# Optimization experiments

Hardware: AMD Instinct MI355X
Metric: run time of the kernel (lower is better)

Reference implementation:

```python
import jax, jax.numpy as jnp
import numpy as np

NUM_HEADS = 8
FOCUSING_FACTOR = 3.0
EPS = 1e-6


def setup_inputs() -> dict:
    key = jax.random.key(0)
    ks = jax.random.split(key, 5)
    B, C, H, W = 16, 256, 64, 64
    hd = C // NUM_HEADS
    return {
        "x": jax.random.normal(ks[0], (B, C, H, W), jnp.float32),
        "qkv_w": jax.random.normal(ks[1], (3 * C, C), jnp.float32) * 0.02,
        "qkv_b": jnp.zeros((3 * C,), jnp.float32),
        "proj_w": jax.random.normal(ks[2], (C, C), jnp.float32) * 0.02,
        "proj_b": jnp.zeros((C,), jnp.float32),
        "dwc_w": jax.random.normal(ks[3], (hd, 1, 5, 5), jnp.float32) * 0.02,
        "dwc_b": jnp.zeros((hd,), jnp.float32),
        "scale": jnp.zeros((1, 1, C), jnp.float32),
    }


def reference(x, qkv_w, qkv_b, proj_w, proj_b, dwc_w, dwc_b, scale):
    B, C, H, W = x.shape
    N = H * W
    hd = C // NUM_HEADS

    # b c h w -> b (h w) c
    xf = x.reshape(B, C, N).transpose(0, 2, 1)
    qkv = xf @ qkv_w.T + qkv_b  # [B, N, 3C]
    q, k, v = jnp.split(qkv, 3, axis=-1)

    # focusing feature map
    q = jax.nn.relu(q) + EPS
    k = jax.nn.relu(k) + EPS
    sc = jax.nn.softplus(scale)
    q = q / sc
    k = k / sc
    q_norm = jnp.linalg.norm(q, axis=-1, keepdims=True)
    k_norm = jnp.linalg.norm(k, axis=-1, keepdims=True)
    # focusing_factor <= 6 branch
    q = q ** FOCUSING_FACTOR
    k = k ** FOCUSING_FACTOR
    q = q / jnp.linalg.norm(q, axis=-1, keepdims=True) * q_norm
    k = k / jnp.linalg.norm(k, axis=-1, keepdims=True) * k_norm

    # b n (h c) -> (b h) n c
    def to_heads(t):
        return t.reshape(B, N, NUM_HEADS, hd).transpose(0, 2, 1, 3).reshape(B * NUM_HEADS, N, hd)

    q, k, v = to_heads(q), to_heads(k), to_heads(v)

    i, j, c, d = N, N, hd, hd
    z = 1.0 / (jnp.einsum('bic,bc->bi', q, k.sum(axis=1)) + EPS)
    if i * j * (c + d) > c * d * (i + j):
        kv = jnp.einsum('bjc,bjd->bcd', k, v)  # [(BH), c, d]
        out = jnp.einsum('bic,bcd,bi->bid', q, kv, z)
    else:
        qk = jnp.einsum('bic,bjc->bij', q, k)
        out = jnp.einsum('bij,bjd,bi->bid', qk, v, z)

    # depthwise conv on v: b (w h) c -> b c w h (square map)
    num = int(N ** 0.5)
    fm = v.transpose(0, 2, 1).reshape(B * NUM_HEADS, hd, num, num)
    fm = jax.lax.conv_general_dilated(
        fm, dwc_w, window_strides=(1, 1), padding='SAME',
        feature_group_count=hd,
        dimension_numbers=('NCHW', 'OIHW', 'NCHW')) + dwc_b[None, :, None, None]
    fm = fm.reshape(B * NUM_HEADS, hd, N).transpose(0, 2, 1)
    out = out + fm

    # (b h) n c -> b n (h c)
    out = out.reshape(B, NUM_HEADS, N, hd).transpose(0, 2, 1, 3).reshape(B, N, C)
    out = out @ proj_w.T + proj_b
    # b (h w) c -> b c h w
    return out.transpose(0, 2, 1).reshape(B, C, H, W)
```

## Files before the change

### kernel.cpp

```cpp
#include <hip/hip_runtime.h>
#include <cmath>

#define B_   16
#define C_   256
#define HW_  64
#define N_   4096
#define NH_  8
#define HD_  32
#define M_   (B_ * N_)
#define QKVC (3 * C_)
#define EPS_ 1e-6f

typedef short bf16x8 __attribute__((ext_vector_type(8)));
typedef float f32x4 __attribute__((ext_vector_type(4)));
typedef unsigned int u32x4 __attribute__((ext_vector_type(4)));

__device__ __forceinline__ float b2f(unsigned short u) {
  union { unsigned int i; float f; } v;
  v.i = ((unsigned int)u) << 16;
  return v.f;
}
__device__ __forceinline__ float blo(unsigned int u) {
  union { unsigned int i; float f; } v; v.i = u << 16; return v.f;
}
__device__ __forceinline__ float bhi(unsigned int u) {
  union { unsigned int i; float f; } v; v.i = u & 0xffff0000u; return v.f;
}
__device__ __forceinline__ unsigned short f2b(float f) {
  union { float f; unsigned int i; } v;
  v.f = f;
  unsigned int r = v.i + 0x7FFFu + ((v.i >> 16) & 1u);
  return (unsigned short)(r >> 16);
}
__device__ __forceinline__ void gload_lds16(const void* g, void* l) {
  __builtin_amdgcn_global_load_lds(
      (const __attribute__((address_space(1))) void*)g,
      (__attribute__((address_space(3))) void*)l, 16, 0, 0);
}

__global__ __launch_bounds__(256) void k_cast_x(const float* __restrict__ x,
                                                unsigned short* __restrict__ xT) {
  __shared__ float t[32][33];
  const int n0 = blockIdx.x * 32, c0 = blockIdx.y * 32, b = blockIdx.z;
  const int tid = threadIdx.x;
  const int r = tid >> 3, g = (tid & 7) * 4;
  float4 v = *reinterpret_cast<const float4*>(
      &x[((size_t)(b * C_ + c0 + r)) * N_ + n0 + g]);
  t[r][g + 0] = v.x; t[r][g + 1] = v.y; t[r][g + 2] = v.z; t[r][g + 3] = v.w;
  __syncthreads();
  ushort4 o;
  o.x = f2b(t[g + 0][r]); o.y = f2b(t[g + 1][r]);
  o.z = f2b(t[g + 2][r]); o.w = f2b(t[g + 3][r]);
  *reinterpret_cast<ushort4*>(&xT[((size_t)(b * N_ + n0 + r)) * C_ + c0 + g]) = o;
}

__global__ __launch_bounds__(256) void k_cast_w(const float* __restrict__ w1,
                                                const float* __restrict__ w2,
                                                unsigned short* __restrict__ dst) {
  const int g4 = (blockIdx.x * 256 + threadIdx.x) * 4;
  float4 v;
  if (g4 < 196608) v = *reinterpret_cast<const float4*>(w1 + g4);
  else             v = *reinterpret_cast<const float4*>(w2 + (g4 - 196608));
  ushort4 o;
  o.x = f2b(v.x); o.y = f2b(v.y); o.z = f2b(v.z); o.w = f2b(v.w);
  *reinterpret_cast<ushort4*>(dst + g4) = o;
}

__global__ void k_prep_scale(const float* __restrict__ scale,
                             float* __restrict__ rsc) {
  const int c = threadIdx.x;
  rsc[c] = 1.f / log1pf(expf(scale[c]));
}

template <int LDA, int OUTMODE, int NCOL>
__global__ __launch_bounds__(256) void k_gemm(
    const unsigned short* __restrict__ A, const unsigned short* __restrict__ W,
    const float* __restrict__ bias, void* __restrict__ outp) {
  __shared__ unsigned short As[128 * 64];
  __shared__ unsigned short Bs[128 * 64];
  const int tid = threadIdx.x;
  const int wid = tid >> 6, lane = tid & 63;
  const int lin = blockIdx.x + blockIdx.y * 512;
  const int bandp = lin >> 3;
  const int rowb = bandp / NCOL;
  const int colb = bandp - rowb * NCOL;
  const int m0 = (((lin & 7) << 6) + rowb) * 128;
  const int col0 = colb * 128;
  const int wr = wid >> 1, wc = wid & 1;

  const int lrow = lane >> 3;
  const int sl = (lane & 7) ^ (lrow & 7);

  f32x4 acc[4][4];
#pragma unroll
  for (int i = 0; i < 4; ++i)
#pragma unroll
    for (int j = 0; j < 4; ++j) acc[i][j] = (f32x4){0.f, 0.f, 0.f, 0.f};

  for (int kt = 0; kt < 4; ++kt) {
    const int k0 = kt * 64;
#pragma unroll
    for (int q = 0; q < 4; ++q) {
      const int chunk = wid * 4 + q;
      const int row = chunk * 8 + lrow;
      gload_lds16(A + (size_t)(m0 + row) * LDA + k0 + sl * 8, &As[chunk * 512]);
      gload_lds16(W + (size_t)(col0 + row) * 256 + k0 + sl * 8, &Bs[chunk * 512]);
    }
    __syncthreads();

    bf16x8 fa[2][4], fb[2][4];
#pragma unroll
    for (int i = 0; i < 4; ++i) {
      const int ra = wr * 64 + i * 16 + (lane & 15);
      const int rb = wc * 64 + i * 16 + (lane & 15);
#pragma unroll
      for (int ks = 0; ks < 2; ++ks) {
        const int s = ks * 4 + (lane >> 4);
        fa[ks][i] = *reinterpret_cast<const bf16x8*>(
            &As[ra * 64 + ((s ^ (ra & 7)) * 8)]);
        fb[ks][i] = *reinterpret_cast<const bf16x8*>(
            &Bs[rb * 64 + ((s ^ (rb & 7)) * 8)]);
      }
    }
#pragma unroll
    for (int i = 0; i < 4; ++i)
#pragma unroll
      for (int j = 0; j < 4; ++j) {
        acc[i][j] = __builtin_amdgcn_mfma_f32_16x16x32_bf16(fa[0][i], fb[0][j],
                                                            acc[i][j], 0, 0, 0);
        acc[i][j] = __builtin_amdgcn_mfma_f32_16x16x32_bf16(fa[1][i], fb[1][j],
                                                            acc[i][j], 0, 0, 0);
      }
    __syncthreads();
  }

  if (OUTMODE == 0) {
    unsigned short* O = (unsigned short*)outp;
#pragma unroll
    for (int j = 0; j < 4; ++j) {
      const int colg = col0 + wc * 64 + j * 16 + (lane & 15);
      const float bb = bias[colg];
#pragma unroll
      for (int i = 0; i < 4; ++i) {
        const int mrow = m0 + wr * 64 + i * 16 + ((lane >> 4) << 2);
#pragma unroll
        for (int r = 0; r < 4; ++r)
          O[(size_t)(mrow + r) * QKVC + colg] = f2b(acc[i][j][r] + bb);
      }
    }
  } else {
    float* O = (float*)outp;
    const int b = m0 >> 12;
    const int nb0 = (m0 & 4095) + wr * 64;
#pragma unroll
    for (int j = 0; j < 4; ++j) {
      const int colg = col0 + wc * 64 + j * 16 + (lane & 15);
      const float bb = bias[colg];
#pragma unroll
      for (int i = 0; i < 4; ++i) {
        const int nb = nb0 + i * 16 + ((lane >> 4) << 2);
        f32x4 o = acc[i][j];
        o += bb;
        __builtin_nontemporal_store(
            o, reinterpret_cast<f32x4*>(&O[((size_t)(b * C_ + colg)) * N_ + nb]));
      }
    }
  }
}

__global__ __launch_bounds__(256) void k_focus(unsigned short* __restrict__ qkv,
                                               const float* __restrict__ rsc) {
  const int wave = threadIdx.x >> 6, lane = threadIdx.x & 63;
  const int t = blockIdx.x * 4 + wave;
  const size_t base = (size_t)t * QKVC + lane * 4;

  uint2 qu = *reinterpret_cast<const uint2*>(qkv + base);
  uint2 ku = *reinterpret_cast<const uint2*>(qkv + base + C_);
  const f32x4 rs = *reinterpret_cast<const f32x4*>(rsc + lane * 4);

  float q[4], k[4], q3[4], k3[4];
  q[0] = blo(qu.x); q[1] = bhi(qu.x); q[2] = blo(qu.y); q[3] = bhi(qu.y);
  k[0] = blo(ku.x); k[1] = bhi(ku.x); k[2] = blo(ku.y); k[3] = bhi(ku.y);

  float sq2 = 0.f, sq6 = 0.f, sk2 = 0.f, sk6 = 0.f;
#pragma unroll
  for (int i = 0; i < 4; ++i) {
    q[i] = (fmaxf(q[i], 0.f) + EPS_) * rs[i];
    k[i] = (fmaxf(k[i], 0.f) + EPS_) * rs[i];
    const float q2 = q[i] * q[i], k2 = k[i] * k[i];
    q3[i] = q2 * q[i];
    k3[i] = k2 * k[i];
    sq2 += q2; sk2 += k2;
    sq6 += q3[i] * q3[i];
    sk6 += k3[i] * k3[i];
  }
#pragma unroll
  for (int off = 1; off < 64; off <<= 1) {
    sq2 += __shfl_xor(sq2, off);
    sq6 += __shfl_xor(sq6, off);
    sk2 += __shfl_xor(sk2, off);
    sk6 += __shfl_xor(sk6, off);
  }
  const float fq = sqrtf(sq2 / sq6);
  const float fk = sqrtf(sk2 / sk6);

  uint2 oq, ok;
  oq.x = (unsigned int)f2b(q3[0] * fq) | ((unsigned int)f2b(q3[1] * fq) << 16);
  oq.y = (unsigned int)f2b(q3[2] * fq) | ((unsigned int)f2b(q3[3] * fq) << 16);
  ok.x = (unsigned int)f2b(k3[0] * fk) | ((unsigned int)f2b(k3[1] * fk) << 16);
  ok.y = (unsigned int)f2b(k3[2] * fk) | ((unsigned int)f2b(k3[3] * fk) << 16);
  *reinterpret_cast<uint2*>(qkv + base) = oq;
  *reinterpret_cast<uint2*>(qkv + base + C_) = ok;
}

__global__ __launch_bounds__(256) void k_kv_part(
    const unsigned short* __restrict__ qkv, float* __restrict__ kvp,
    float* __restrict__ ksp) {
  const int bh = blockIdx.x;
  const int chunk = blockIdx.y;
  const int b = bh >> 3, h = bh & 7;
  const int tid = threadIdx.x;
  const int wave = tid >> 6;
  __shared__ unsigned short ks[2][64 * 32];
  __shared__ unsigned short vs[2][64 * 32];

  const int c = tid >> 3;
  const int d0 = (tid & 7) * 4;
  const int row = tid >> 2;
  const int seg = (tid & 3) * 8;
  const int j0 = chunk * 512;

  float a0 = 0.f, a1 = 0.f, a2 = 0.f, a3 = 0.f, ksum_acc = 0.f;

#define KV_STAGE(buf, jt)                                                     \
  {                                                                           \
    const size_t rb =                                                         \
        ((size_t)(b * N_ + (jt) + row)) * QKVC + h * HD_ + seg;               \
    gload_lds16(qkv + rb + C_, &ks[buf][wave * 512]);                         \
    gload_lds16(qkv + rb + 2 * C_, &vs[buf][wave * 512]);                     \
  }

  KV_STAGE(0, j0);
  __syncthreads();

  int cur = 0;
  for (int t = 0; t < 8; ++t) {
    if (t < 7) KV_STAGE(cur ^ 1, j0 + (t + 1) * 64);
#pragma unroll 8
    for (int jj = 0; jj < 64; ++jj) {
      const float kc = b2f(ks[cur][jj * 32 + c]);
      const uint2 vv =
          *reinterpret_cast<const uint2*>(&vs[cur][jj * 32 + d0]);
      a0 += kc * blo(vv.x);
      a1 += kc * bhi(vv.x);
      a2 += kc * blo(vv.y);
      a3 += kc * bhi(vv.y);
      ksum_acc += kc;
    }
    __syncthreads();
    cur ^= 1;
  }
#undef KV_STAGE

  float* kvo = kvp + ((size_t)chunk * 128 + bh) * 1024 + c * 32 + d0;
  kvo[0] = a0; kvo[1] = a1; kvo[2] = a2; kvo[3] = a3;
  if ((tid & 7) == 0) ksp[((size_t)chunk * 128 + bh) * 32 + c] = ksum_acc;
}

__global__ __launch_bounds__(256) void k_attn_mfma(
    unsigned short* __restrict__ qkv, const float* __restrict__ kvp,
    const float* __restrict__ ksp) {
  const int bh = blockIdx.y;
  const int b = bh >> 3, h = bh & 7;
  const int tid = threadIdx.x;
  const int lane = tid & 63;
  const int r0 = blockIdx.x * 256 + (tid >> 6) * 64;

  __shared__ float kv_s[1024];
  __shared__ float ksum_s[32];
  for (int pp = tid; pp < 1024; pp += 256) {
    float s = 0.f;
#pragma unroll
    for (int ch = 0; ch < 8; ++ch)
      s += kvp[((size_t)ch * 128 + bh) * 1024 + pp];
    kv_s[pp] = s;
  }
  if (tid < 32) {
    float s = 0.f;
#pragma unroll
    for (int ch = 0; ch < 8; ++ch)
      s += ksp[((size_t)ch * 128 + bh) * 32 + tid];
    ksum_s[tid] = s;
  }
  __syncthreads();

  const int kb = (lane >> 4) * 8;
  const int col = lane & 15;
  bf16x8 bhi0, bhi1, blo0, blo1;
  float ks0[8];
#pragma unroll
  for (int t = 0; t < 8; ++t) {
    const float v0 = kv_s[(kb + t) * 32 + col];
    const float v1 = kv_s[(kb + t) * 32 + col + 16];
    const unsigned short h0 = f2b(v0), h1 = f2b(v1);
    ((unsigned short*)&bhi0)[t] = h0;
    ((unsigned short*)&bhi1)[t] = h1;
    ((unsigned short*)&blo0)[t] = f2b(v0 - b2f(h0));
    ((unsigned short*)&blo1)[t] = f2b(v1 - b2f(h1));
    ks0[t] = ksum_s[kb + t];
  }

#pragma unroll
  for (int rt = 0; rt < 4; ++rt) {
    const int row = r0 + rt * 16 + (lane & 15);
    const bf16x8 a = *reinterpret_cast<const bf16x8*>(
        qkv + (size_t)(b * N_ + row) * QKVC + h * HD_ + kb);
    float zp = 0.f;
#pragma unroll
    for (int t = 0; t < 8; ++t) zp += b2f(((const unsigned short*)&a)[t]) * ks0[t];
    zp += __shfl_xor(zp, 16);
    zp += __shfl_xor(zp, 32);
    const float z = 1.f / (zp + EPS_);

    f32x4 acc0 = {0.f, 0.f, 0.f, 0.f}, acc1 = {0.f, 0.f, 0.f, 0.f};
    acc0 = __builtin_amdgcn_mfma_f32_16x16x32_bf16(a, blo0, acc0, 0, 0, 0);
    acc1 = __builtin_amdgcn_mfma_f32_16x16x32_bf16(a, blo1, acc1, 0, 0, 0);
    acc0 = __builtin_amdgcn_mfma_f32_16x16x32_bf16(a, bhi0, acc0, 0, 0, 0);
    acc1 = __builtin_amdgcn_mfma_f32_16x16x32_bf16(a, bhi1, acc1, 0, 0, 0);

#pragma unroll
    for (int r = 0; r < 4; ++r) {
      const int rr = (lane >> 4) * 4 + r;
      const float zr = __shfl(z, rr);
      unsigned short* op =
          qkv + (size_t)(b * N_ + r0 + rt * 16 + rr) * QKVC + h * HD_;
      op[col] = f2b(acc0[r] * zr);
      op[col + 16] = f2b(acc1[r] * zr);
    }
  }
}

__global__ __launch_bounds__(256) void k_conv(
    unsigned short* __restrict__ qkv, const float* __restrict__ dwc_w,
    const float* __restrict__ dwc_b) {
  const int lin = blockIdx.x;
  const int g2 = (lin & 7) * 256 + (lin >> 3);
  const int bh = g2 >> 4;
  const int ig = g2 & 15;
  const int i0 = ig * 4;
  const int b = bh >> 3, h = bh & 7;
  const int tid = threadIdx.x;
  const int j = tid >> 2;
  const int g = tid & 3;
  const int d0 = g * 8;
  const int wave = tid >> 6, lane = tid & 63;

  __shared__ float w_s[800];
  __shared__ float b_s[32];
  __shared__ unsigned short v_s[8 * 64 * 32];

#pragma unroll
  for (int rr = 0; rr < 8; ++rr) {
    const int ii = i0 + rr - 2;
    if (ii < 0 || ii >= 64) continue;
    gload_lds16(qkv + ((size_t)(b * N_ + ii * 64 + wave * 16 + (lane >> 2))) * QKVC +
                    2 * C_ + h * HD_ + (lane & 3) * 8,
                &v_s[rr * 2048 + wave * 512]);
  }
  for (int p = tid; p < 800; p += 256)
    w_s[p] = dwc_w[(p & 31) * 25 + (p >> 5)];
  if (tid < 32) b_s[tid] = dwc_b[tid];
  __syncthreads();

#pragma unroll
  for (int r = 0; r < 4; ++r) {
    const int i = i0 + r;
    float fm[8];
#pragma unroll
    for (int dd = 0; dd < 8; ++dd) fm[dd] = b_s[d0 + dd];
#pragma unroll
    for (int kr = 0; kr < 5; ++kr) {
      const int ii = i + kr - 2;
      if (ii < 0 || ii >= 64) continue;
      const int lr = r + kr;
#pragma unroll
      for (int kj = 0; kj < 5; ++kj) {
        const int jj = j + kj - 2;
        if (jj < 0 || jj >= 64) continue;
        const unsigned int* vr = reinterpret_cast<const unsigned int*>(
            &v_s[lr * 2048 + jj * 32 + d0]);
        const float* wt = &w_s[(kr * 5 + kj) * 32 + d0];
#pragma unroll
        for (int p = 0; p < 4; ++p) {
          const unsigned int vu = vr[p];
          fm[2 * p + 0] += blo(vu) * wt[2 * p + 0];
          fm[2 * p + 1] += bhi(vu) * wt[2 * p + 1];
        }
      }
    }
    unsigned int* orow = reinterpret_cast<unsigned int*>(
        qkv + ((size_t)(b * N_ + i * 64 + j)) * QKVC + h * HD_ + d0);
    uint4 cur = *reinterpret_cast<const uint4*>(orow);
    unsigned int o[4] = {cur.x, cur.y, cur.z, cur.w};
#pragma unroll
    for (int p = 0; p < 4; ++p) {
      const unsigned int lo = f2b(blo(o[p]) + fm[2 * p + 0]);
      const unsigned int hi = f2b(bhi(o[p]) + fm[2 * p + 1]);
      o[p] = lo | (hi << 16);
    }
    *reinterpret_cast<uint4*>(orow) = make_uint4(o[0], o[1], o[2], o[3]);
  }
}

extern "C" void kernel_launch(void* const* d_in, const int* in_sizes, int n_in,
                              void* d_out, int out_size, void* d_ws,
                              size_t ws_size, hipStream_t stream) {
  (void)in_sizes; (void)n_in; (void)out_size; (void)ws_size;
  const float* x      = (const float*)d_in[0];
  const float* qkv_w  = (const float*)d_in[1];
  const float* qkv_b  = (const float*)d_in[2];
  const float* proj_w = (const float*)d_in[3];
  const float* proj_b = (const float*)d_in[4];
  const float* dwc_w  = (const float*)d_in[5];
  const float* dwc_b  = (const float*)d_in[6];
  const float* scale  = (const float*)d_in[7];
  float* out = (float*)d_out;

  char* w = (char*)d_ws;
  unsigned short* xT   = (unsigned short*)w; w += (size_t)M_ * C_ * 2;
  unsigned short* qkvb = (unsigned short*)w; w += (size_t)M_ * QKVC * 2;
  unsigned short* wq   = (unsigned short*)w; w += (size_t)(QKVC + C_) * C_ * 2;
  unsigned short* wp   = wq + (size_t)QKVC * C_;
  float* kvp   = (float*)w;                  w += (size_t)8 * 128 * 1024 * 4;
  float* ksp   = (float*)w;                  w += (size_t)8 * 128 * 32 * 4;
  float* rscb  = (float*)w;                  w += 256 * 4;

  k_prep_scale<<<1, 256, 0, stream>>>(scale, rscb);
  k_cast_x<<<dim3(N_ / 32, C_ / 32, B_), 256, 0, stream>>>(x, xT);
  k_cast_w<<<256, 256, 0, stream>>>(qkv_w, proj_w, wq);
  k_gemm<256, 0, 6><<<dim3(512, 6), 256, 0, stream>>>(
      xT, wq, qkv_b, (void*)qkvb);
  k_focus<<<M_ / 4, 256, 0, stream>>>(qkvb, rscb);
  k_kv_part<<<dim3(128, 8), 256, 0, stream>>>(qkvb, kvp, ksp);
  k_attn_mfma<<<dim3(N_ / 256, 128), 256, 0, stream>>>(qkvb, kvp, ksp);
  k_conv<<<2048, 256, 0, stream>>>(qkvb, dwc_w, dwc_b);
  k_gemm<768, 1, 2><<<dim3(512, 2), 256, 0, stream>>>(
      qkvb, wp, proj_b, (void*)out);
}
```

Baseline: 217.5 us.

## Rework KV partial reduction with fp32 padded LDS and more chunks

The k_kv_part kernel now splits the sequence into 16 chunks instead of 8, doubling grid parallelism. Staging moves from async bf16 global-to-LDS copies to register-prefetched loads that are converted to fp32 and stored in padded LDS rows, so the inner loop skips bf16 unpacking and avoids bank conflicts. The attention kernel reduces over 16 partials instead of 8. The cost is more partial-sum traffic, a larger workspace and a single LDS buffer with an extra barrier per tile.

```diff
diff --git a/kernel.cpp b/kernel.cpp
--- a/kernel.cpp
+++ b/kernel.cpp
@@ -213,6 +213,7 @@
   *reinterpret_cast<uint2*>(qkv + base + C_) = ok;
 }
 
+#define KVP_CHUNKS 16
 __global__ __launch_bounds__(256) void k_kv_part(
     const unsigned short* __restrict__ qkv, float* __restrict__ kvp,
     float* __restrict__ ksp) {
@@ -220,51 +221,58 @@
   const int chunk = blockIdx.y;
   const int b = bh >> 3, h = bh & 7;
   const int tid = threadIdx.x;
-  const int wave = tid >> 6;
-  __shared__ unsigned short ks[2][64 * 32];
-  __shared__ unsigned short vs[2][64 * 32];
+  __shared__ float ksf[64 * 36];
+  __shared__ float vsf[64 * 36];
 
   const int c = tid >> 3;
   const int d0 = (tid & 7) * 4;
-  const int row = tid >> 2;
-  const int seg = (tid & 3) * 8;
-  const int j0 = chunk * 512;
-
-  float a0 = 0.f, a1 = 0.f, a2 = 0.f, a3 = 0.f, ksum_acc = 0.f;
-
-#define KV_STAGE(buf, jt)                                                     \
-  {                                                                           \
-    const size_t rb =                                                         \
-        ((size_t)(b * N_ + (jt) + row)) * QKVC + h * HD_ + seg;               \
-    gload_lds16(qkv + rb + C_, &ks[buf][wave * 512]);                         \
-    gload_lds16(qkv + rb + 2 * C_, &vs[buf][wave * 512]);                     \
-  }
-
-  KV_STAGE(0, j0);
-  __syncthreads();
-
-  int cur = 0;
-  for (int t = 0; t < 8; ++t) {
-    if (t < 7) KV_STAGE(cur ^ 1, j0 + (t + 1) * 64);
+  const int srow = tid >> 2;
+  const int sseg = (tid & 3) * 8;
+  const int j0 = chunk * 256;
+
+  float a0 = 0.f, a1 = 0.f, a2 = 0.f, a3 = 0.f, ksum = 0.f;
+
+  uint4 ku, vu;
+  {
+    const size_t rb = ((size_t)(b * N_ + j0 + srow)) * QKVC + h * HD_ + sseg;
+    ku = *reinterpret_cast<const uint4*>(qkv + rb + C_);
+    vu = *reinterpret_cast<const uint4*>(qkv + rb + 2 * C_);
+  }
+
+  for (int t = 0; t < 4; ++t) {
+    {
+      f32x4 k0 = {blo(ku.x), bhi(ku.x), blo(ku.y), bhi(ku.y)};
+      f32x4 k1 = {blo(ku.z), bhi(ku.z), blo(ku.w), bhi(ku.w)};
+      f32x4 v0 = {blo(vu.x), bhi(vu.x), blo(vu.y), bhi(vu.y)};
+      f32x4 v1 = {blo(vu.z), bhi(vu.z), blo(vu.w), bhi(vu.w)};
+      *reinterpret_cast<f32x4*>(&ksf[srow * 36 + sseg]) = k0;
+      *reinterpret_cast<f32x4*>(&ksf[srow * 36 + sseg + 4]) = k1;
+      *reinterpret_cast<f32x4*>(&vsf[srow * 36 + sseg]) = v0;
+      *reinterpret_cast<f32x4*>(&vsf[srow * 36 + sseg + 4]) = v1;
+    }
+    __syncthreads();
+    if (t < 3) {
+      const size_t rb =
+          ((size_t)(b * N_ + j0 + (t + 1) * 64 + srow)) * QKVC + h * HD_ + sseg;
+      ku = *reinterpret_cast<const uint4*>(qkv + rb + C_);
+      vu = *reinterpret_cast<const uint4*>(qkv + rb + 2 * C_);
+    }
 #pragma unroll 8
     for (int jj = 0; jj < 64; ++jj) {
-      const float kc = b2f(ks[cur][jj * 32 + c]);
-      const uint2 vv =
-          *reinterpret_cast<const uint2*>(&vs[cur][jj * 32 + d0]);
-      a0 += kc * blo(vv.x);
-      a1 += kc * bhi(vv.x);
-      a2 += kc * blo(vv.y);
-      a3 += kc * bhi(vv.y);
-      ksum_acc += kc;
+      const float kc = ksf[jj * 36 + c];
+      const f32x4 vv = *reinterpret_cast<const f32x4*>(&vsf[jj * 36 + d0]);
+      a0 += kc * vv[0];
+      a1 += kc * vv[1];
+      a2 += kc * vv[2];
+      a3 += kc * vv[3];
+      ksum += kc;
     }
     __syncthreads();
-    cur ^= 1;
-  }
-#undef KV_STAGE
+  }
 
   float* kvo = kvp + ((size_t)chunk * 128 + bh) * 1024 + c * 32 + d0;
   kvo[0] = a0; kvo[1] = a1; kvo[2] = a2; kvo[3] = a3;
-  if ((tid & 7) == 0) ksp[((size_t)chunk * 128 + bh) * 32 + c] = ksum_acc;
+  if ((tid & 7) == 0) ksp[((size_t)chunk * 128 + bh) * 32 + c] = ksum;
 }
 
 __global__ __launch_bounds__(256) void k_attn_mfma(
@@ -281,14 +289,14 @@
   for (int pp = tid; pp < 1024; pp += 256) {
     float s = 0.f;
 #pragma unroll
-    for (int ch = 0; ch < 8; ++ch)
+    for (int ch = 0; ch < KVP_CHUNKS; ++ch)
       s += kvp[((size_t)ch * 128 + bh) * 1024 + pp];
     kv_s[pp] = s;
   }
   if (tid < 32) {
     float s = 0.f;
 #pragma unroll
-    for (int ch = 0; ch < 8; ++ch)
+    for (int ch = 0; ch < KVP_CHUNKS; ++ch)
       s += ksp[((size_t)ch * 128 + bh) * 32 + tid];
     ksum_s[tid] = s;
   }
@@ -431,8 +439,8 @@
   unsigned short* qkvb = (unsigned short*)w; w += (size_t)M_ * QKVC * 2;
   unsigned short* wq   = (unsigned short*)w; w += (size_t)(QKVC + C_) * C_ * 2;
   unsigned short* wp   = wq + (size_t)QKVC * C_;
-  float* kvp   = (float*)w;                  w += (size_t)8 * 128 * 1024 * 4;
-  float* ksp   = (float*)w;                  w += (size_t)8 * 128 * 32 * 4;
+  float* kvp   = (float*)w;                  w += (size_t)KVP_CHUNKS * 128 * 1024 * 4;
+  float* ksp   = (float*)w;                  w += (size_t)KVP_CHUNKS * 128 * 32 * 4;
   float* rscb  = (float*)w;                  w += 256 * 4;
 
   k_prep_scale<<<1, 256, 0, stream>>>(scale, rscb);
@@ -441,7 +449,7 @@
   k_gemm<256, 0, 6><<<dim3(512, 6), 256, 0, stream>>>(
       xT, wq, qkv_b, (void*)qkvb);
   k_focus<<<M_ / 4, 256, 0, stream>>>(qkvb, rscb);
-  k_kv_part<<<dim3(128, 8), 256, 0, stream>>>(qkvb, kvp, ksp);
+  k_kv_part<<<dim3(128, KVP_CHUNKS), 256, 0, stream>>>(qkvb, kvp, ksp);
   k_attn_mfma<<<dim3(N_ / 256, 128), 256, 0, stream>>>(qkvb, kvp, ksp);
   k_conv<<<2048, 256, 0, stream>>>(qkvb, dwc_w, dwc_b);
   k_gemm<768, 1, 2><<<dim3(512, 2), 256, 0, stream>>>(
```

Result: faster. 210.7 us (-3.1%).
